# Performance work log

Hardware: AMD Instinct MI355X
Metric: run time of the kernel (lower is better)

## Reference

```python
import jax, jax.numpy as jnp
import numpy as np

SPARSITY_RATIO = 0.1


def setup_inputs() -> dict:
    key = jax.random.key(0)
    ks = jax.random.split(key, 11)
    B, S, d = 4, 2048, 16  # d = n_sparse_dims + 2
    inp = {
        "full": jax.random.normal(ks[0], (B, S, d), dtype=jnp.float32),
        "sw1": jax.random.normal(ks[1], (d, 32), dtype=jnp.float32) * 0.1,
        "sb1": jax.random.normal(ks[2], (32,), dtype=jnp.float32) * 0.1,
        "sw2": jax.random.normal(ks[3], (32, 1), dtype=jnp.float32) * 0.1,
        "sb2": jax.random.normal(ks[4], (1,), dtype=jnp.float32) * 0.1,
        "mw1": jax.random.normal(ks[5], (3 * d, 64), dtype=jnp.float32) * 0.1,
        "mb1": jax.random.normal(ks[6], (64,), dtype=jnp.float32) * 0.1,
        "mw2": jax.random.normal(ks[7], (64, 32), dtype=jnp.float32) * 0.1,
        "mb2": jax.random.normal(ks[8], (32,), dtype=jnp.float32) * 0.1,
        "mw3": jax.random.normal(ks[9], (32, d), dtype=jnp.float32) * 0.1,
        "mb3": jax.random.normal(ks[10], (d,), dtype=jnp.float32) * 0.1,
    }
    return inp


def reference(full, sw1, sb1, sw2, sb2, mw1, mb1, mw2, mb2, mw3, mb3):
    B, S, d = full.shape
    k = max(1, int(S * SPARSITY_RATIO))  # static python int

    # importance scores: Linear(d,32) -> ReLU -> Linear(32,1)
    scores = (jax.nn.relu(full @ sw1 + sb1) @ sw2 + sb2)[..., 0]  # [B, S]
    _, top_idx = jax.lax.top_k(scores, k)  # [B, k]

    # gather selected tokens (keys == values)
    sel = jnp.take_along_axis(full, top_idx[:, :, None], axis=1)  # [B, k, d]

    # First MLP layer on concat([q, keys, values]) decomposed to avoid the
    # [B,S,k,3d] concat: mw1 splits into query / key / value blocks.
    w_q, w_k, w_v = mw1[:d], mw1[d:2 * d], mw1[2 * d:]
    q_part = full @ w_q                     # [B, S, 64]
    kv_part = sel @ (w_k + w_v)             # [B, k, 64]
    h1 = jax.nn.relu(q_part[:, :, None, :] + kv_part[:, None, :, :] + mb1)  # [B,S,k,64]
    h2 = jax.nn.relu(h1 @ mw2 + mb2)        # [B, S, k, 32]
    out = h2 @ mw3 + mb3                    # [B, S, k, d]
    return out.mean(axis=2)                 # [B, S, d]
```

## Files before the change

### kernel.cpp

```cpp
#include <hip/hip_runtime.h>
#include <hip/hip_bf16.h>

#define BB 4
#define SS 2048
#define DD 16
#define KK 204

typedef __attribute__((ext_vector_type(8))) short short8;
typedef __attribute__((ext_vector_type(4))) float f32x4;

__device__ inline short f2bf(float x) {
  __hip_bfloat16 b = __float2bfloat16(x);
  return *reinterpret_cast<short*>(&b);
}

__global__ void __launch_bounds__(128) score_kernel(
    const float* __restrict__ full, const float* __restrict__ sw1,
    const float* __restrict__ sb1, const float* __restrict__ sw2,
    const float* __restrict__ sb2, float* __restrict__ scores_g) {
  __shared__ float swT[32][16];
  __shared__ float sb1s[32], sw2s[32];
  int t = threadIdx.x;
#pragma unroll
  for (int it = 0; it < 4; it++) {
    int idx = t + it * 128;
    int n = idx & 31, k = idx >> 5;
    swT[n][k] = sw1[k * 32 + n];
  }
  if (t < 32) { sb1s[t] = sb1[t]; sw2s[t] = sw2[t]; }

  int row = blockIdx.x * 128 + t;
  const float* xp = full + row * DD;
  f32x4 x0 = *(const f32x4*)(xp);
  f32x4 x1 = *(const f32x4*)(xp + 4);
  f32x4 x2 = *(const f32x4*)(xp + 8);
  f32x4 x3 = *(const f32x4*)(xp + 12);
  __syncthreads();

  float sc = sb2[0];
#pragma unroll
  for (int n = 0; n < 32; n++) {
    const f32x4* wp = (const f32x4*)&swT[n][0];
    f32x4 w0 = wp[0], w1 = wp[1], w2 = wp[2], w3 = wp[3];
    float a = sb1s[n];
#pragma unroll
    for (int k = 0; k < 4; k++) a += x0[k] * w0[k];
#pragma unroll
    for (int k = 0; k < 4; k++) a += x1[k] * w1[k];
#pragma unroll
    for (int k = 0; k < 4; k++) a += x2[k] * w2[k];
#pragma unroll
    for (int k = 0; k < 4; k++) a += x3[k] * w3[k];
    sc += fmaxf(a, 0.f) * sw2s[n];
  }
  scores_g[row] = sc;
}

__global__ void __launch_bounds__(1024) mega_kernel(
    const float* __restrict__ full, const float* __restrict__ mw1,
    const float* __restrict__ mb1, const float* __restrict__ mw2,
    const float* __restrict__ mb2, const float* __restrict__ mw3,
    const float* __restrict__ mb3, const float* __restrict__ scores_g,
    float* __restrict__ out) {
  int bs_base = blockIdx.x * 32;
  int b = bs_base >> 11;
  int t = threadIdx.x;
  int w = t >> 6;
  int l = t & 63;
  int mt = w >> 3;
  int wl = w & 7;
  int ml = l & 15;
  int g = l >> 4;

  __shared__ float s_kvb[KK * 64];
  __shared__ float qs[32 * 64];
  __shared__ float xs[32 * 16];
  __shared__ float s_xsel[KK * DD];
  __shared__ int s_idx[KK];
  __shared__ int wtot[16];
  __shared__ unsigned long long s_pfx;
  __shared__ int s_r;
  int* hist = (int*)s_kvb;
  float (*red)[512] = (float(*)[512])s_kvb;

  unsigned long long key[2];
#pragma unroll
  for (int e = 0; e < 2; e++) {
    int i = t + e * 1024;
    unsigned u = __float_as_uint(scores_g[b * SS + i]);
    u = (u & 0x80000000u) ? ~u : (u | 0x80000000u);
    key[e] = ((unsigned long long)u << 11) | (unsigned)(SS - 1 - i);
  }
  if (t < 512) xs[t] = full[bs_base * DD + t];
  if (t == 0) { s_pfx = 0ull; s_r = KK; }
  __syncthreads();

  {
    int r = t >> 5, n = t & 31;
    float q0 = 0.f, q1 = 0.f;
#pragma unroll
    for (int k = 0; k < 16; k++) {
      float xv = xs[r * 16 + k];
      q0 += xv * mw1[k * 64 + n];
      q1 += xv * mw1[k * 64 + n + 32];
    }
    qs[r * 64 + n] = q0;
    qs[r * 64 + n + 32] = q1;
  }

  for (int pass = 0; pass < 4; pass++) {
    int s = 33 - pass * 11;
    hist[t] = 0;
    hist[t + 1024] = 0;
    __syncthreads();
    unsigned long long pfx = s_pfx;
    int r = s_r;
#pragma unroll
    for (int e = 0; e < 2; e++)
      if ((key[e] >> (s + 11)) == pfx)
        atomicAdd(&hist[(int)((key[e] >> s) & 0x7FF)], 1);
    __syncthreads();
    int loc0 = hist[2 * t], loc1 = hist[2 * t + 1];
    int ls0 = loc0 + loc1, ls1 = loc1;
    int tot = ls0;
    int incl = tot;
#pragma unroll
    for (int off = 1; off < 64; off <<= 1) {
      int o = __shfl_down(incl, off);
      incl += (l + off < 64) ? o : 0;
    }
    if (l == 0) wtot[w] = incl;
    __syncthreads();
    int waveoff = 0;
    for (int ww = w + 1; ww < 16; ww++) waveoff += wtot[ww];
    int excl = waveoff + (incl - tot);
    int sufs0 = ls0 + excl, sufs1 = ls1 + excl;
    if (sufs0 >= r && sufs1 < r) {
      s_pfx = (pfx << 11) | (unsigned)(2 * t);
      s_r = r - sufs1;
    }
    if (sufs1 >= r && excl < r) {
      s_pfx = (pfx << 11) | (unsigned)(2 * t + 1);
      s_r = r - excl;
    }
    __syncthreads();
  }

  unsigned long long kstar = s_pfx;
  bool sel0 = (key[0] >= kstar), sel1 = (key[1] >= kstar);
  int c = (sel0 ? 1 : 0) + (sel1 ? 1 : 0);
  int p = c;
#pragma unroll
  for (int off = 1; off < 64; off <<= 1) {
    int o = __shfl_up(p, off);
    p += (l >= off) ? o : 0;
  }
  if (l == 63) wtot[w] = p;
  __syncthreads();
  int base = 0;
  for (int ww = 0; ww < w; ww++) base += wtot[ww];
  int pos = base + p - c;
  if (sel0) s_idx[pos++] = t;
  if (sel1) s_idx[pos] = t + 1024;
  __syncthreads();

  {
    f32x4* dst = (f32x4*)s_xsel;
    for (int i = t; i < KK * 4; i += 1024) {
      int j = i >> 2, qu = i & 3;
      dst[i] = ((const f32x4*)(full + (b * SS + s_idx[j]) * DD))[qu];
    }
  }
  float wreg[16];
#pragma unroll
  for (int k = 0; k < 16; k++)
    wreg[k] = mw1[(16 + k) * 64 + l] + mw1[(32 + k) * 64 + l];
  float biasv = mb1[l];
  __syncthreads();

  for (int j = w; j < KK; j += 16) {
    const f32x4* xr = (const f32x4*)(s_xsel + j * DD);
    f32x4 x0 = xr[0], x1 = xr[1], x2 = xr[2], x3 = xr[3];
    float a = biasv;
#pragma unroll
    for (int k = 0; k < 4; k++) a += x0[k] * wreg[k];
#pragma unroll
    for (int k = 0; k < 4; k++) a += x1[k] * wreg[4 + k];
#pragma unroll
    for (int k = 0; k < 4; k++) a += x2[k] * wreg[8 + k];
#pragma unroll
    for (int k = 0; k < 4; k++) a += x3[k] * wreg[12 + k];
    s_kvb[j * 64 + l] = a;
  }

  short8 bfrag[2][2];
#pragma unroll
  for (int nt = 0; nt < 2; nt++)
#pragma unroll
    for (int kh = 0; kh < 2; kh++)
#pragma unroll
      for (int i = 0; i < 8; i++) {
        int k = kh * 32 + 8 * g + i;
        bfrag[nt][kh][i] = f2bf(mw2[k * 32 + nt * 16 + ml]);
      }
  f32x4 biasfrag[2];
#pragma unroll
  for (int nt = 0; nt < 2; nt++) {
    float bv = mb2[nt * 16 + ml];
    f32x4 bf;
    bf[0] = bv; bf[1] = bv; bf[2] = bv; bf[3] = bv;
    biasfrag[nt] = bf;
  }
  f32x4 qv[2][2];
  {
    const float* qp = qs + (mt * 16 + ml) * 64 + 8 * g;
    qv[0][0] = *(const f32x4*)(qp);
    qv[0][1] = *(const f32x4*)(qp + 4);
    qv[1][0] = *(const f32x4*)(qp + 32);
    qv[1][1] = *(const f32x4*)(qp + 36);
  }
  __syncthreads();

  float accs[2][4] = {};
  int jbeg = wl * 26;
  int jend = jbeg + 26;
  if (jend > KK) jend = KK;
  const float* kvbl = s_kvb + 8 * g;
#pragma unroll 2
  for (int j = jbeg; j < jend; j++) {
    const float* kp = kvbl + j * 64;
    f32x4 kv[2][2];
    kv[0][0] = *(const f32x4*)(kp);
    kv[0][1] = *(const f32x4*)(kp + 4);
    kv[1][0] = *(const f32x4*)(kp + 32);
    kv[1][1] = *(const f32x4*)(kp + 36);

    short8 afrag[2];
#pragma unroll
    for (int kh = 0; kh < 2; kh++)
#pragma unroll
      for (int hf = 0; hf < 2; hf++)
#pragma unroll
        for (int i = 0; i < 4; i++) {
          float h = fmaxf(qv[kh][hf][i] + kv[kh][hf][i], 0.f);
          afrag[kh][hf * 4 + i] = f2bf(h);
        }

#pragma unroll
    for (int nt = 0; nt < 2; nt++) {
      f32x4 cacc = __builtin_amdgcn_mfma_f32_16x16x32_bf16(
          afrag[0], bfrag[nt][0], biasfrag[nt], 0, 0, 0);
      cacc = __builtin_amdgcn_mfma_f32_16x16x32_bf16(
          afrag[1], bfrag[nt][1], cacc, 0, 0, 0);
#pragma unroll
      for (int r = 0; r < 4; r++) accs[nt][r] += fmaxf(cacc[r], 0.f);
    }
  }

  __syncthreads();
#pragma unroll
  for (int nt = 0; nt < 2; nt++)
#pragma unroll
    for (int r = 0; r < 4; r++)
      red[w][(4 * g + r) * 32 + nt * 16 + ml] = accs[nt][r];
  __syncthreads();
  {
    int h = t >> 9, cidx = t & 511;
    float sum = 0.f;
#pragma unroll
    for (int ww = 0; ww < 8; ww++) sum += red[h * 8 + ww][cidx];
    sum *= (1.0f / (float)KK);
    red[h * 8][cidx] = sum;
  }
  __syncthreads();

  if (t < 512) {
    int mt_e = t >> 8, tl = t & 255;
    int m = tl >> 4, dc = tl & 15;
    float o = mb3[dc];
#pragma unroll
    for (int n = 0; n < 32; n++) o += red[mt_e * 8][m * 32 + n] * mw3[n * 16 + dc];
    out[(bs_base + mt_e * 16 + m) * 16 + dc] = o;
  }
}

extern "C" void kernel_launch(void* const* d_in, const int* in_sizes, int n_in,
                              void* d_out, int out_size, void* d_ws, size_t ws_size,
                              hipStream_t stream) {
  const float* full = (const float*)d_in[0];
  const float* sw1  = (const float*)d_in[1];
  const float* sb1  = (const float*)d_in[2];
  const float* sw2  = (const float*)d_in[3];
  const float* sb2  = (const float*)d_in[4];
  const float* mw1  = (const float*)d_in[5];
  const float* mb1  = (const float*)d_in[6];
  const float* mw2  = (const float*)d_in[7];
  const float* mb2  = (const float*)d_in[8];
  const float* mw3  = (const float*)d_in[9];
  const float* mb3  = (const float*)d_in[10];
  float* out = (float*)d_out;

  float* scores_g = (float*)d_ws;

  score_kernel<<<64, 128, 0, stream>>>(full, sw1, sb1, sw2, sb2, scores_g);
  mega_kernel<<<BB * SS / 32, 1024, 0, stream>>>(full, mw1, mb1, mw2, mb2, mw3,
                                                 mb3, scores_g, out);
}
```

Before: 36.73 us.

## Run top-k radix select in a single wavefront to eliminate block barriers

The 4-pass radix select over the 2048 score keys now runs inside wave 0 only. Keys are staged in shared memory and the histogram uses a swizzled layout so each lane can scan 32 contiguous bins. This replaces the many block-wide __syncthreads and cross-wave scans per pass with wave-level shuffles and a ballot. The trade-off is that one wave does 32 atomics and reads per lane per pass while the other 15 waves sit idle, and the selected-row gather and kv projection are moved after the select.

Result: slower. 43.36 us (+18.0%).

```diff
diff --git a/kernel.cpp b/kernel.cpp
--- a/kernel.cpp
+++ b/kernel.cpp
@@ -5,6 +5,7 @@
 #define SS 2048
 #define DD 16
 #define KK 204
+#define HADDR(bb) ((((bb) & 63) << 5) | ((bb) >> 6))
 
 typedef __attribute__((ext_vector_type(8))) short short8;
 typedef __attribute__((ext_vector_type(4))) float f32x4;
@@ -77,22 +78,19 @@
   __shared__ float xs[32 * 16];
   __shared__ float s_xsel[KK * DD];
   __shared__ int s_idx[KK];
-  __shared__ int wtot[16];
-  __shared__ unsigned long long s_pfx;
-  __shared__ int s_r;
   int* hist = (int*)s_kvb;
+  unsigned long long* s_keys =
+      (unsigned long long*)(s_kvb + 2048);
   float (*red)[512] = (float(*)[512])s_kvb;
 
-  unsigned long long key[2];
 #pragma unroll
   for (int e = 0; e < 2; e++) {
     int i = t + e * 1024;
     unsigned u = __float_as_uint(scores_g[b * SS + i]);
     u = (u & 0x80000000u) ? ~u : (u | 0x80000000u);
-    key[e] = ((unsigned long long)u << 11) | (unsigned)(SS - 1 - i);
+    s_keys[i] = ((unsigned long long)u << 11) | (unsigned)(SS - 1 - i);
   }
   if (t < 512) xs[t] = full[bs_base * DD + t];
-  if (t == 0) { s_pfx = 0ull; s_r = KK; }
   __syncthreads();
 
   {
@@ -107,90 +105,61 @@
     qs[r * 64 + n] = q0;
     qs[r * 64 + n + 32] = q1;
   }
-
-  for (int pass = 0; pass < 4; pass++) {
-    int s = 33 - pass * 11;
-    hist[t] = 0;
-    hist[t + 1024] = 0;
-    __syncthreads();
-    unsigned long long pfx = s_pfx;
-    int r = s_r;
-#pragma unroll
-    for (int e = 0; e < 2; e++)
-      if ((key[e] >> (s + 11)) == pfx)
-        atomicAdd(&hist[(int)((key[e] >> s) & 0x7FF)], 1);
-    __syncthreads();
-    int loc0 = hist[2 * t], loc1 = hist[2 * t + 1];
-    int ls0 = loc0 + loc1, ls1 = loc1;
-    int tot = ls0;
-    int incl = tot;
+  __syncthreads();
+
+  if (w == 0) {
+    unsigned long long pfx = 0ull;
+    int r = KK;
+    for (int pass = 0; pass < 4; pass++) {
+      int s = 33 - pass * 11;
+#pragma unroll
+      for (int z = 0; z < 32; z++) hist[l + 64 * z] = 0;
+      for (int e = 0; e < 32; e++) {
+        unsigned long long ke = s_keys[l + 64 * e];
+        if ((ke >> (s + 11)) == pfx)
+          atomicAdd(&hist[HADDR((int)((ke >> s) & 0x7FF))], 1);
+      }
+      int tot = 0;
+#pragma unroll
+      for (int z = 0; z < 32; z++) tot += hist[HADDR(l * 32 + z)];
+      int incl = tot;
+#pragma unroll
+      for (int off = 1; off < 64; off <<= 1) {
+        int o = __shfl_down(incl, off);
+        incl += (l + off < 64) ? o : 0;
+      }
+      int sufn = incl - tot;
+      long long fpfx = -1;
+      int fr = 0;
+      for (int z = 31; z >= 0; z--) {
+        int cnt = hist[HADDR(l * 32 + z)];
+        int sufs = sufn + cnt;
+        if (sufs >= r && sufn < r) {
+          fpfx = (long long)((pfx << 11) | (unsigned)(l * 32 + z));
+          fr = r - sufn;
+        }
+        sufn = sufs;
+      }
+      unsigned long long bal = __ballot(fpfx >= 0);
+      int src = __ffsll((long long)bal) - 1;
+      pfx = (unsigned long long)__shfl((long long)fpfx, src);
+      r = __shfl(fr, src);
+    }
+    unsigned long long kstar = pfx;
+    unsigned selmask = 0u;
+    int c = 0;
+    for (int e = 0; e < 32; e++) {
+      if (s_keys[l + 64 * e] >= kstar) { selmask |= (1u << e); c++; }
+    }
+    int p = c;
 #pragma unroll
     for (int off = 1; off < 64; off <<= 1) {
-      int o = __shfl_down(incl, off);
-      incl += (l + off < 64) ? o : 0;
-    }
-    if (l == 0) wtot[w] = incl;
-    __syncthreads();
-    int waveoff = 0;
-    for (int ww = w + 1; ww < 16; ww++) waveoff += wtot[ww];
-    int excl = waveoff + (incl - tot);
-    int sufs0 = ls0 + excl, sufs1 = ls1 + excl;
-    if (sufs0 >= r && sufs1 < r) {
-      s_pfx = (pfx << 11) | (unsigned)(2 * t);
-      s_r = r - sufs1;
-    }
-    if (sufs1 >= r && excl < r) {
-      s_pfx = (pfx << 11) | (unsigned)(2 * t + 1);
-      s_r = r - excl;
-    }
-    __syncthreads();
-  }
-
-  unsigned long long kstar = s_pfx;
-  bool sel0 = (key[0] >= kstar), sel1 = (key[1] >= kstar);
-  int c = (sel0 ? 1 : 0) + (sel1 ? 1 : 0);
-  int p = c;
-#pragma unroll
-  for (int off = 1; off < 64; off <<= 1) {
-    int o = __shfl_up(p, off);
-    p += (l >= off) ? o : 0;
-  }
-  if (l == 63) wtot[w] = p;
-  __syncthreads();
-  int base = 0;
-  for (int ww = 0; ww < w; ww++) base += wtot[ww];
-  int pos = base + p - c;
-  if (sel0) s_idx[pos++] = t;
-  if (sel1) s_idx[pos] = t + 1024;
-  __syncthreads();
-
-  {
-    f32x4* dst = (f32x4*)s_xsel;
-    for (int i = t; i < KK * 4; i += 1024) {
-      int j = i >> 2, qu = i & 3;
-      dst[i] = ((const f32x4*)(full + (b * SS + s_idx[j]) * DD))[qu];
-    }
-  }
-  float wreg[16];
-#pragma unroll
-  for (int k = 0; k < 16; k++)
-    wreg[k] = mw1[(16 + k) * 64 + l] + mw1[(32 + k) * 64 + l];
-  float biasv = mb1[l];
-  __syncthreads();
-
-  for (int j = w; j < KK; j += 16) {
-    const f32x4* xr = (const f32x4*)(s_xsel + j * DD);
-    f32x4 x0 = xr[0], x1 = xr[1], x2 = xr[2], x3 = xr[3];
-    float a = biasv;
-#pragma unroll
-    for (int k = 0; k < 4; k++) a += x0[k] * wreg[k];
-#pragma unroll
-    for (int k = 0; k < 4; k++) a += x1[k] * wreg[4 + k];
-#pragma unroll
-    for (int k = 0; k < 4; k++) a += x2[k] * wreg[8 + k];
-#pragma unroll
-    for (int k = 0; k < 4; k++) a += x3[k] * wreg[12 + k];
-    s_kvb[j * 64 + l] = a;
+      int o = __shfl_up(p, off);
+      p += (l >= off) ? o : 0;
+    }
+    int pos = p - c;
+    for (int e = 0; e < 32; e++)
+      if (selmask & (1u << e)) s_idx[pos++] = l + 64 * e;
   }
 
   short8 bfrag[2][2];
@@ -218,6 +187,36 @@
     qv[0][1] = *(const f32x4*)(qp + 4);
     qv[1][0] = *(const f32x4*)(qp + 32);
     qv[1][1] = *(const f32x4*)(qp + 36);
+  }
+  float wreg[16];
+#pragma unroll
+  for (int k = 0; k < 16; k++)
+    wreg[k] = mw1[(16 + k) * 64 + l] + mw1[(32 + k) * 64 + l];
+  float biasv = mb1[l];
+  __syncthreads();
+
+  {
+    f32x4* dst = (f32x4*)s_xsel;
+    for (int i = t; i < KK * 4; i += 1024) {
+      int j = i >> 2, qu = i & 3;
+      dst[i] = ((const f32x4*)(full + (b * SS + s_idx[j]) * DD))[qu];
+    }
+  }
+  __syncthreads();
+
+  for (int j = w; j < KK; j += 16) {
+    const f32x4* xr = (const f32x4*)(s_xsel + j * DD);
+    f32x4 x0 = xr[0], x1 = xr[1], x2 = xr[2], x3 = xr[3];
+    float a = biasv;
+#pragma unroll
+    for (int k = 0; k < 4; k++) a += x0[k] * wreg[k];
+#pragma unroll
+    for (int k = 0; k < 4; k++) a += x1[k] * wreg[4 + k];
+#pragma unroll
+    for (int k = 0; k < 4; k++) a += x2[k] * wreg[8 + k];
+#pragma unroll
+    for (int k = 0; k < 4; k++) a += x3[k] * wreg[12 + k];
+    s_kvb[j * 64 + l] = a;
   }
   __syncthreads();
 
```
